# Kernel tuning notes

Hardware: AMD Instinct MI355X
Metric: run time of the kernel (lower is better)

## Reference

```python
import jax, jax.numpy as jnp
import numpy as np

N = 50000      # nodes
E = 800000     # edges (avg degree 16)
F_IN = 256
F_OUT = 256


def setup_inputs() -> dict:
    key = jax.random.key(0)
    ks = jax.random.split(key, 8)
    feature = jax.random.normal(ks[0], (N, F_IN), dtype=jnp.float32)
    e_w = jax.random.uniform(ks[1], (E, 1), dtype=jnp.float32)
    snorm_n = jnp.ones((N, 1), dtype=jnp.float32)
    snorm_e = jnp.ones((E, 1), dtype=jnp.float32)
    src = jax.random.randint(ks[2], (E,), 0, N, dtype=jnp.int32)
    dst = jax.random.randint(ks[3], (E,), 0, N, dtype=jnp.int32)
    scale = 1.0 / np.sqrt(F_IN)
    W_self = jax.random.normal(ks[4], (F_IN, F_OUT), dtype=jnp.float32) * scale
    W = jax.random.normal(ks[5], (F_IN, F_OUT), dtype=jnp.float32) * scale
    b = jax.random.normal(ks[6], (F_OUT,), dtype=jnp.float32) * scale
    return {"feature": feature, "e_w": e_w, "snorm_n": snorm_n,
            "snorm_e": snorm_e, "W_self": W_self, "W": W, "b": b,
            "src": src, "dst": dst}


def reference(feature, e_w, snorm_n, snorm_e, W_self, W, b, src, dst):
    n = feature.shape[0]
    ones_e = jnp.ones_like(src, dtype=feature.dtype)
    # self transform
    h_s = feature @ W_self                                   # [N, F_OUT]
    # source-side degree normalization: deg_out^{-1/2}
    out_deg = jnp.maximum(jax.ops.segment_sum(ones_e, src, num_segments=n), 1.0)
    feat = feature * (out_deg ** -0.5)[:, None]              # [N, F_IN]
    # message = h[src] * e_w, aggregated by sum into dst (u_mul_e + sum reduce)
    msgs = feat[src] * e_w                                   # [E, F_IN]
    agg = jax.ops.segment_sum(msgs, dst, num_segments=n)     # [N, F_IN]
    # neighbor transform + destination-side degree normalization
    h = agg @ W + b                                          # [N, F_OUT]
    in_deg = jnp.maximum(jax.ops.segment_sum(ones_e, dst, num_segments=n), 1.0)
    h = h * (in_deg ** -0.5)[:, None]
    return h_s + h, e_w
```

## Files before the change

### kernel.cpp

```cpp
#include <hip/hip_runtime.h>
#include <hip/hip_bf16.h>

#define N_NODES 50000
#define N_EDGES 800000
#define MP      50048
#define MAXDEG  64

#define PREP_A_BLOCKS 12512
#define EDGE_BLOCKS   3125
#define PREPW_BLOCKS  512

typedef __bf16 bf16x8_t __attribute__((ext_vector_type(8)));
typedef float  f32x4_t  __attribute__((ext_vector_type(4)));

__device__ __forceinline__ unsigned short f2bf(float x) {
  __hip_bfloat16 h = __float2bfloat16(x);
  return __builtin_bit_cast(unsigned short, h);
}
__device__ __forceinline__ float bf2f(unsigned short u) {
  unsigned int v = ((unsigned int)u) << 16;
  return __builtin_bit_cast(float, v);
}

__global__ __launch_bounds__(256) void prep_fused(
    const float* __restrict__ feature, const float* __restrict__ Wself,
    const float* __restrict__ W, const float* __restrict__ e_w,
    const int* __restrict__ src, const int* __restrict__ dst,
    unsigned short* __restrict__ Abf, unsigned short* __restrict__ Bt,
    int* __restrict__ cnt_in, int* __restrict__ cnt_out,
    unsigned int* __restrict__ bucket, float* __restrict__ out1)
{
  const int b = blockIdx.x, tid = threadIdx.x;
  if (b < PREP_A_BLOCKS) {
    int idx4 = b * 256 + tid;
    size_t base = (size_t)idx4 * 4;
    int row = (int)(base >> 8);
    ushort4 o;
    if (row < N_NODES) {
      const float4 v = *(const float4*)(feature + base);
      o.x = f2bf(v.x); o.y = f2bf(v.y); o.z = f2bf(v.z); o.w = f2bf(v.w);
    } else {
      o.x = o.y = o.z = o.w = 0;
    }
    *(ushort4*)(Abf + base) = o;
  } else if (b < PREP_A_BLOCKS + EDGE_BLOCKS) {
    int e = (b - PREP_A_BLOCKS) * 256 + tid;
    if (e < N_EDGES) {
      int s = src[e];
      int d = dst[e];
      float w = e_w[e];
      out1[e] = w;
      atomicAdd(&cnt_out[s], 1);
      int p = atomicAdd(&cnt_in[d], 1);
      if (p < MAXDEG) {
        unsigned int ent = ((unsigned int)f2bf(w) << 16) | (unsigned int)s;
        bucket[(size_t)d * MAXDEG + p] = ent;
      }
    }
  } else {
    int idx = (b - (PREP_A_BLOCKS + EDGE_BLOCKS)) * 256 + tid;
    int n = idx >> 8, k = idx & 255;
    float v = (n < 256) ? Wself[k * 256 + n] : W[k * 256 + (n - 256)];
    Bt[idx] = f2bf(v);
  }
}

__global__ __launch_bounds__(256, 2) void gemm_kernel(
    const unsigned short* __restrict__ A,
    const unsigned short* __restrict__ Bt,
    const float* __restrict__ bias,
    const int* __restrict__ cnt_in,
    const int* __restrict__ cnt_out,
    float* __restrict__ out0,
    unsigned char* __restrict__ y8)
{
  __shared__ unsigned short As[2][128 * 32];
  __shared__ unsigned short Bs[2][256 * 32];
  const int tid  = threadIdx.x;
  const int lane = tid & 63;
  const int wave = tid >> 6;
  const int m0 = blockIdx.x * 128;
  const int n0 = blockIdx.y * 256;
  const int wm = (wave & 1) * 64;
  const int wn = (wave >> 1) * 128;
  const int fr = lane & 15;
  const int fk = (lane >> 4) * 8;
  const int srow  = lane >> 2;
  const int scolb = (lane & 3) * 8;

  f32x4_t acc[4][8] = {};

  for (int k0 = 0; k0 < 256; k0 += 64) {
#pragma unroll
    for (int p = 0; p < 2; ++p) {
      int kk = k0 + p * 32;
#pragma unroll
      for (int j = 0; j < 2; ++j) {
        int rr = wave * 32 + j * 16;
        const unsigned short* ga = A + (size_t)(m0 + rr + srow) * 256 + (kk + scolb);
        __builtin_amdgcn_global_load_lds((const __attribute__((address_space(1))) void*)ga,
                                         (__attribute__((address_space(3))) void*)&As[p][rr * 32],
                                         16, 0, 0);
      }
#pragma unroll
      for (int j = 0; j < 4; ++j) {
        int rr = wave * 64 + j * 16;
        const unsigned short* gb = Bt + (size_t)(n0 + rr + srow) * 256 + (kk + scolb);
        __builtin_amdgcn_global_load_lds((const __attribute__((address_space(1))) void*)gb,
                                         (__attribute__((address_space(3))) void*)&Bs[p][rr * 32],
                                         16, 0, 0);
      }
    }
    __syncthreads();

#pragma unroll
    for (int p = 0; p < 2; ++p) {
      bf16x8_t af[4], bfr[8];
#pragma unroll
      for (int i = 0; i < 4; ++i)
        af[i]  = *(const bf16x8_t*)&As[p][(wm + i * 16 + fr) * 32 + fk];
#pragma unroll
      for (int j = 0; j < 8; ++j)
        bfr[j] = *(const bf16x8_t*)&Bs[p][(wn + j * 16 + fr) * 32 + fk];
#pragma unroll
      for (int i = 0; i < 4; ++i)
#pragma unroll
        for (int j = 0; j < 8; ++j)
          acc[i][j] = __builtin_amdgcn_mfma_f32_16x16x32_bf16(af[i], bfr[j], acc[i][j], 0, 0, 0);
    }
    __syncthreads();
  }

  if (blockIdx.y == 0) {
#pragma unroll
    for (int i = 0; i < 4; ++i) {
      int rowb = m0 + wm + i * 16 + (lane >> 4) * 4;
      float indv[4];
#pragma unroll
      for (int r = 0; r < 4; ++r) {
        int row = rowb + r;
        if (row < N_NODES) {
          int ci = cnt_in[row]; if (ci < 1) ci = 1;
          indv[r] = rsqrtf((float)ci);
        } else indv[r] = 0.f;
      }
#pragma unroll
      for (int j = 0; j < 8; ++j) {
        int col = wn + j * 16 + (lane & 15);
        float bc = bias[col];
#pragma unroll
        for (int r = 0; r < 4; ++r) {
          int row = rowb + r;
          if (row < N_NODES)
            out0[(size_t)row * 256 + col] = acc[i][j][r] + bc * indv[r];
        }
      }
    }
  } else {
#pragma unroll
    for (int i = 0; i < 4; ++i) {
      int rowb = m0 + wm + i * 16 + (lane >> 4) * 4;
      float odv[4];
#pragma unroll
      for (int r = 0; r < 4; ++r) {
        int row = rowb + r;
        if (row < N_NODES) {
          int co = cnt_out[row]; if (co < 1) co = 1;
          odv[r] = rsqrtf((float)co);
        } else odv[r] = 0.f;
      }
#pragma unroll
      for (int j = 0; j < 8; ++j) {
        int col = wn + j * 16 + (lane & 15);
#pragma unroll
        for (int r = 0; r < 4; ++r) {
          int row = rowb + r;
          if (row < N_NODES) {
            float ys = acc[i][j][r] * odv[r];
            unsigned int pk = (unsigned int)__builtin_amdgcn_cvt_pk_fp8_f32(ys, ys, 0, false);
            y8[(size_t)row * 256 + col] = (unsigned char)(pk & 0xffu);
          }
        }
      }
    }
  }
}

__global__ __launch_bounds__(256) void agg_kernel(
    const unsigned char* __restrict__ y8, const unsigned int* __restrict__ bucket,
    const int* __restrict__ cnt_in, float* __restrict__ out0)
{
  const int wave = threadIdx.x >> 6, lane = threadIdx.x & 63;
  const int node = blockIdx.x * 4 + wave;
  if (node >= N_NODES) return;
  int deg_raw = cnt_in[node];
  int deg = deg_raw > MAXDEG ? MAXDEG : deg_raw;

  unsigned int ent = 0u;
  if (lane < deg) ent = bucket[(size_t)node * MAXDEG + lane];
  float wl = bf2f((unsigned short)(ent >> 16));
  int   sl = (int)(ent & 0xffffu);

  float a0 = 0.f, a1 = 0.f, a2 = 0.f, a3 = 0.f;
  for (int b = 0; b < MAXDEG; b += 16) {
    if (b >= deg) break;
#pragma unroll
    for (int t = 0; t < 16; ++t) {
      int eb = b + t;
      int   s = __shfl(sl, eb);
      float w = __shfl(wl, eb);
      bool ok = eb < deg;
      s = ok ? s : 0;
      w = ok ? w : 0.0f;
      unsigned int u = *(const unsigned int*)(y8 + (size_t)s * 256 + lane * 4);
      a0 += w * __builtin_amdgcn_cvt_f32_fp8(u, 0);
      a1 += w * __builtin_amdgcn_cvt_f32_fp8(u, 1);
      a2 += w * __builtin_amdgcn_cvt_f32_fp8(u, 2);
      a3 += w * __builtin_amdgcn_cvt_f32_fp8(u, 3);
    }
  }

  int dn = deg_raw < 1 ? 1 : deg_raw;
  float inv = rsqrtf((float)dn);
  float4 o = *(float4*)(out0 + (size_t)node * 256 + lane * 4);
  o.x += a0 * inv; o.y += a1 * inv; o.z += a2 * inv; o.w += a3 * inv;
  *(float4*)(out0 + (size_t)node * 256 + lane * 4) = o;
}

extern "C" void kernel_launch(void* const* d_in, const int* in_sizes, int n_in,
                              void* d_out, int out_size, void* d_ws, size_t ws_size,
                              hipStream_t stream) {
  const float* feature = (const float*)d_in[0];
  const float* e_w     = (const float*)d_in[1];
  const float* W_self  = (const float*)d_in[4];
  const float* W       = (const float*)d_in[5];
  const float* bias    = (const float*)d_in[6];
  const int*   src     = (const int*)d_in[7];
  const int*   dst     = (const int*)d_in[8];

  float* out0 = (float*)d_out;
  float* out1 = out0 + (size_t)N_NODES * 256;

  char* ws = (char*)d_ws;
  int*            cnt_in  = (int*)(ws + 0);
  int*            cnt_out = (int*)(ws + 204800);
  unsigned int*   bucket  = (unsigned int*)(ws + 409600);
  unsigned short* Bt      = (unsigned short*)(ws + 13209600);
  unsigned short* Abf     = (unsigned short*)(ws + 13471744);
  unsigned char*  y8      = (unsigned char*)(ws + 39096320);

  hipMemsetAsync(ws, 0, 409600, stream);

  prep_fused<<<PREP_A_BLOCKS + EDGE_BLOCKS + PREPW_BLOCKS, 256, 0, stream>>>(
      feature, W_self, W, e_w, src, dst, Abf, Bt, cnt_in, cnt_out, bucket, out1);
  gemm_kernel<<<dim3(MP / 128, 2), 256, 0, stream>>>(Abf, Bt, bias, cnt_in, cnt_out, out0, y8);
  agg_kernel<<<(N_NODES + 3) / 4, 256, 0, stream>>>(y8, bucket, cnt_in, out0);
}
```

Baseline: 264.2 us.

## Fuse feature bf16 conversion into GEMM and run edge pass in same launch

The separate pass that converts feature to bf16 is removed. The GEMM now loads fp32 feature rows directly into registers and converts them there. The edge bucketing pass runs as extra blocks of the same launch, so degree counting overlaps the GEMM. Because degrees are not final during the GEMM, the neighbor half is written unscaled as bf16, and a new scale_y8 kernel applies the out-degree scaling and fp8 packing; bias moves into the aggregation kernel. This saves the Abf write and reread but adds a bf16 intermediate pass, one extra launch and uncoalesced direct A loads.

```diff
diff --git a/kernel.cpp b/kernel.cpp
--- a/kernel.cpp
+++ b/kernel.cpp
@@ -6,12 +6,12 @@
 #define MP      50048
 #define MAXDEG  64
 
-#define PREP_A_BLOCKS 12512
-#define EDGE_BLOCKS   3125
-#define PREPW_BLOCKS  512
+#define EDGE_BLOCKS 3125
+#define GEMM_BLOCKS 782
 
 typedef __bf16 bf16x8_t __attribute__((ext_vector_type(8)));
 typedef float  f32x4_t  __attribute__((ext_vector_type(4)));
+typedef unsigned short ushort8_t __attribute__((ext_vector_type(8)));
 
 __device__ __forceinline__ unsigned short f2bf(float x) {
   __hip_bfloat16 h = __float2bfloat16(x);
@@ -22,65 +22,51 @@
   return __builtin_bit_cast(float, v);
 }
 
-__global__ __launch_bounds__(256) void prep_fused(
-    const float* __restrict__ feature, const float* __restrict__ Wself,
-    const float* __restrict__ W, const float* __restrict__ e_w,
+__global__ __launch_bounds__(256) void prep_W(
+    const float* __restrict__ Wself, const float* __restrict__ W,
+    unsigned short* __restrict__ Bt)
+{
+  int idx = blockIdx.x * 256 + threadIdx.x;
+  int n = idx >> 8, k = idx & 255;
+  float v = (n < 256) ? Wself[k * 256 + n] : W[k * 256 + (n - 256)];
+  Bt[idx] = f2bf(v);
+}
+
+__global__ __launch_bounds__(256, 2) void mega_kernel(
+    const float* __restrict__ feature,
+    const float* __restrict__ e_w,
     const int* __restrict__ src, const int* __restrict__ dst,
-    unsigned short* __restrict__ Abf, unsigned short* __restrict__ Bt,
+    const unsigned short* __restrict__ Bt,
     int* __restrict__ cnt_in, int* __restrict__ cnt_out,
-    unsigned int* __restrict__ bucket, float* __restrict__ out1)
-{
-  const int b = blockIdx.x, tid = threadIdx.x;
-  if (b < PREP_A_BLOCKS) {
-    int idx4 = b * 256 + tid;
-    size_t base = (size_t)idx4 * 4;
-    int row = (int)(base >> 8);
-    ushort4 o;
-    if (row < N_NODES) {
-      const float4 v = *(const float4*)(feature + base);
-      o.x = f2bf(v.x); o.y = f2bf(v.y); o.z = f2bf(v.z); o.w = f2bf(v.w);
-    } else {
-      o.x = o.y = o.z = o.w = 0;
-    }
-    *(ushort4*)(Abf + base) = o;
-  } else if (b < PREP_A_BLOCKS + EDGE_BLOCKS) {
-    int e = (b - PREP_A_BLOCKS) * 256 + tid;
-    if (e < N_EDGES) {
-      int s = src[e];
-      int d = dst[e];
-      float w = e_w[e];
-      out1[e] = w;
-      atomicAdd(&cnt_out[s], 1);
-      int p = atomicAdd(&cnt_in[d], 1);
-      if (p < MAXDEG) {
-        unsigned int ent = ((unsigned int)f2bf(w) << 16) | (unsigned int)s;
-        bucket[(size_t)d * MAXDEG + p] = ent;
-      }
-    }
-  } else {
-    int idx = (b - (PREP_A_BLOCKS + EDGE_BLOCKS)) * 256 + tid;
-    int n = idx >> 8, k = idx & 255;
-    float v = (n < 256) ? Wself[k * 256 + n] : W[k * 256 + (n - 256)];
-    Bt[idx] = f2bf(v);
-  }
-}
-
-__global__ __launch_bounds__(256, 2) void gemm_kernel(
-    const unsigned short* __restrict__ A,
-    const unsigned short* __restrict__ Bt,
-    const float* __restrict__ bias,
-    const int* __restrict__ cnt_in,
-    const int* __restrict__ cnt_out,
+    unsigned int* __restrict__ bucket, float* __restrict__ out1,
     float* __restrict__ out0,
-    unsigned char* __restrict__ y8)
-{
-  __shared__ unsigned short As[2][128 * 32];
+    unsigned short* __restrict__ zraw)
+{
+  const int bid = blockIdx.x;
+  const int tid = threadIdx.x;
+
+  if (bid < EDGE_BLOCKS) {
+    int e = bid * 256 + tid;
+    int s = src[e];
+    int d = dst[e];
+    float w = e_w[e];
+    out1[e] = w;
+    atomicAdd(&cnt_out[s], 1);
+    int p = atomicAdd(&cnt_in[d], 1);
+    if (p < MAXDEG) {
+      unsigned int ent = ((unsigned int)f2bf(w) << 16) | (unsigned int)s;
+      bucket[(size_t)d * MAXDEG + p] = ent;
+    }
+    return;
+  }
+
   __shared__ unsigned short Bs[2][256 * 32];
-  const int tid  = threadIdx.x;
+  const int gb = bid - EDGE_BLOCKS;
+  const int m0 = (gb >> 1) * 128;
+  const int nhalf = gb & 1;
+  const int n0 = nhalf * 256;
   const int lane = tid & 63;
   const int wave = tid >> 6;
-  const int m0 = blockIdx.x * 128;
-  const int n0 = blockIdx.y * 256;
   const int wm = (wave & 1) * 64;
   const int wn = (wave >> 1) * 128;
   const int fr = lane & 15;
@@ -95,30 +81,39 @@
     for (int p = 0; p < 2; ++p) {
       int kk = k0 + p * 32;
 #pragma unroll
-      for (int j = 0; j < 2; ++j) {
-        int rr = wave * 32 + j * 16;
-        const unsigned short* ga = A + (size_t)(m0 + rr + srow) * 256 + (kk + scolb);
-        __builtin_amdgcn_global_load_lds((const __attribute__((address_space(1))) void*)ga,
-                                         (__attribute__((address_space(3))) void*)&As[p][rr * 32],
-                                         16, 0, 0);
-      }
-#pragma unroll
       for (int j = 0; j < 4; ++j) {
         int rr = wave * 64 + j * 16;
-        const unsigned short* gb = Bt + (size_t)(n0 + rr + srow) * 256 + (kk + scolb);
-        __builtin_amdgcn_global_load_lds((const __attribute__((address_space(1))) void*)gb,
+        const unsigned short* gbp = Bt + (size_t)(n0 + rr + srow) * 256 + (kk + scolb);
+        __builtin_amdgcn_global_load_lds((const __attribute__((address_space(1))) void*)gbp,
                                          (__attribute__((address_space(3))) void*)&Bs[p][rr * 32],
                                          16, 0, 0);
       }
     }
+
+    bf16x8_t af[2][4];
+#pragma unroll
+    for (int p = 0; p < 2; ++p) {
+      int kk = k0 + p * 32;
+#pragma unroll
+      for (int i = 0; i < 4; ++i) {
+        int row = m0 + wm + i * 16 + fr;
+        const float* ap = feature + (size_t)row * 256 + kk + fk;
+        float4 lo = make_float4(0.f, 0.f, 0.f, 0.f), hi = lo;
+        if (row < N_NODES) {
+          lo = *(const float4*)ap;
+          hi = *(const float4*)(ap + 4);
+        }
+        ushort8_t u;
+        u[0] = f2bf(lo.x); u[1] = f2bf(lo.y); u[2] = f2bf(lo.z); u[3] = f2bf(lo.w);
+        u[4] = f2bf(hi.x); u[5] = f2bf(hi.y); u[6] = f2bf(hi.z); u[7] = f2bf(hi.w);
+        af[p][i] = __builtin_bit_cast(bf16x8_t, u);
+      }
+    }
     __syncthreads();
 
 #pragma unroll
     for (int p = 0; p < 2; ++p) {
-      bf16x8_t af[4], bfr[8];
-#pragma unroll
-      for (int i = 0; i < 4; ++i)
-        af[i]  = *(const bf16x8_t*)&As[p][(wm + i * 16 + fr) * 32 + fk];
+      bf16x8_t bfr[8];
 #pragma unroll
       for (int j = 0; j < 8; ++j)
         bfr[j] = *(const bf16x8_t*)&Bs[p][(wn + j * 16 + fr) * 32 + fk];
@@ -126,33 +121,23 @@
       for (int i = 0; i < 4; ++i)
 #pragma unroll
         for (int j = 0; j < 8; ++j)
-          acc[i][j] = __builtin_amdgcn_mfma_f32_16x16x32_bf16(af[i], bfr[j], acc[i][j], 0, 0, 0);
+          acc[i][j] = __builtin_amdgcn_mfma_f32_16x16x32_bf16(af[p][i], bfr[j], acc[i][j], 0, 0, 0);
     }
     __syncthreads();
   }
 
-  if (blockIdx.y == 0) {
+  if (nhalf == 0) {
 #pragma unroll
     for (int i = 0; i < 4; ++i) {
       int rowb = m0 + wm + i * 16 + (lane >> 4) * 4;
-      float indv[4];
-#pragma unroll
-      for (int r = 0; r < 4; ++r) {
-        int row = rowb + r;
-        if (row < N_NODES) {
-          int ci = cnt_in[row]; if (ci < 1) ci = 1;
-          indv[r] = rsqrtf((float)ci);
-        } else indv[r] = 0.f;
-      }
 #pragma unroll
       for (int j = 0; j < 8; ++j) {
         int col = wn + j * 16 + (lane & 15);
-        float bc = bias[col];
 #pragma unroll
         for (int r = 0; r < 4; ++r) {
           int row = rowb + r;
           if (row < N_NODES)
-            out0[(size_t)row * 256 + col] = acc[i][j][r] + bc * indv[r];
+            out0[(size_t)row * 256 + col] = acc[i][j][r];
         }
       }
     }
@@ -160,35 +145,51 @@
 #pragma unroll
     for (int i = 0; i < 4; ++i) {
       int rowb = m0 + wm + i * 16 + (lane >> 4) * 4;
-      float odv[4];
-#pragma unroll
-      for (int r = 0; r < 4; ++r) {
-        int row = rowb + r;
-        if (row < N_NODES) {
-          int co = cnt_out[row]; if (co < 1) co = 1;
-          odv[r] = rsqrtf((float)co);
-        } else odv[r] = 0.f;
-      }
 #pragma unroll
       for (int j = 0; j < 8; ++j) {
         int col = wn + j * 16 + (lane & 15);
 #pragma unroll
         for (int r = 0; r < 4; ++r) {
           int row = rowb + r;
-          if (row < N_NODES) {
-            float ys = acc[i][j][r] * odv[r];
-            unsigned int pk = (unsigned int)__builtin_amdgcn_cvt_pk_fp8_f32(ys, ys, 0, false);
-            y8[(size_t)row * 256 + col] = (unsigned char)(pk & 0xffu);
-          }
+          if (row < N_NODES)
+            zraw[(size_t)row * 256 + col] = f2bf(acc[i][j][r]);
         }
       }
     }
   }
+}
+
+__global__ __launch_bounds__(256) void scale_y8(
+    const unsigned short* __restrict__ zraw, const int* __restrict__ cnt_out,
+    unsigned char* __restrict__ y8)
+{
+  int idx = blockIdx.x * 256 + threadIdx.x;
+  int row = idx >> 4;
+  size_t eo = (size_t)idx * 16;
+  int co = cnt_out[row]; if (co < 1) co = 1;
+  float s = rsqrtf((float)co);
+  const ushort8_t* zp = (const ushort8_t*)(zraw + eo);
+  ushort8_t z0 = zp[0], z1 = zp[1];
+  float v[16];
+#pragma unroll
+  for (int t = 0; t < 8; ++t) { v[t] = bf2f(z0[t]) * s; v[8 + t] = bf2f(z1[t]) * s; }
+  uint4 o;
+  unsigned int d;
+  d = (unsigned int)__builtin_amdgcn_cvt_pk_fp8_f32(v[0],  v[1],  0u, false);
+  o.x = (unsigned int)__builtin_amdgcn_cvt_pk_fp8_f32(v[2],  v[3],  d,  true);
+  d = (unsigned int)__builtin_amdgcn_cvt_pk_fp8_f32(v[4],  v[5],  0u, false);
+  o.y = (unsigned int)__builtin_amdgcn_cvt_pk_fp8_f32(v[6],  v[7],  d,  true);
+  d = (unsigned int)__builtin_amdgcn_cvt_pk_fp8_f32(v[8],  v[9],  0u, false);
+  o.z = (unsigned int)__builtin_amdgcn_cvt_pk_fp8_f32(v[10], v[11], d,  true);
+  d = (unsigned int)__builtin_amdgcn_cvt_pk_fp8_f32(v[12], v[13], 0u, false);
+  o.w = (unsigned int)__builtin_amdgcn_cvt_pk_fp8_f32(v[14], v[15], d,  true);
+  *(uint4*)(y8 + eo) = o;
 }
 
 __global__ __launch_bounds__(256) void agg_kernel(
     const unsigned char* __restrict__ y8, const unsigned int* __restrict__ bucket,
-    const int* __restrict__ cnt_in, float* __restrict__ out0)
+    const int* __restrict__ cnt_in, const float* __restrict__ bias,
+    float* __restrict__ out0)
 {
   const int wave = threadIdx.x >> 6, lane = threadIdx.x & 63;
   const int node = blockIdx.x * 4 + wave;
@@ -222,8 +223,12 @@
 
   int dn = deg_raw < 1 ? 1 : deg_raw;
   float inv = rsqrtf((float)dn);
+  float4 bv = *(const float4*)(bias + lane * 4);
   float4 o = *(float4*)(out0 + (size_t)node * 256 + lane * 4);
-  o.x += a0 * inv; o.y += a1 * inv; o.z += a2 * inv; o.w += a3 * inv;
+  o.x += (a0 + bv.x) * inv;
+  o.y += (a1 + bv.y) * inv;
+  o.z += (a2 + bv.z) * inv;
+  o.w += (a3 + bv.w) * inv;
   *(float4*)(out0 + (size_t)node * 256 + lane * 4) = o;
 }
 
@@ -246,13 +251,14 @@
   int*            cnt_out = (int*)(ws + 204800);
   unsigned int*   bucket  = (unsigned int*)(ws + 409600);
   unsigned short* Bt      = (unsigned short*)(ws + 13209600);
-  unsigned short* Abf     = (unsigned short*)(ws + 13471744);
+  unsigned short* zraw    = (unsigned short*)(ws + 13471744);
   unsigned char*  y8      = (unsigned char*)(ws + 39096320);
 
   hipMemsetAsync(ws, 0, 409600, stream);
 
-  prep_fused<<<PREP_A_BLOCKS + EDGE_BLOCKS + PREPW_BLOCKS, 256, 0, stream>>>(
-      feature, W_self, W, e_w, src, dst, Abf, Bt, cnt_in, cnt_out, bucket, out1);
-  gemm_kernel<<<dim3(MP / 128, 2), 256, 0, stream>>>(Abf, Bt, bias, cnt_in, cnt_out, out0, y8);
-  agg_kernel<<<(N_NODES + 3) / 4, 256, 0, stream>>>(y8, bucket, cnt_in, out0);
-}
+  prep_W<<<512, 256, 0, stream>>>(W_self, W, Bt);
+  mega_kernel<<<EDGE_BLOCKS + GEMM_BLOCKS, 256, 0, stream>>>(
+      feature, e_w, src, dst, Bt, cnt_in, cnt_out, bucket, out1, out0, zraw);
+  scale_y8<<<3125, 256, 0, stream>>>(zraw, cnt_out, y8);
+  agg_kernel<<<(N_NODES + 3) / 4, 256, 0, stream>>>(y8, bucket, cnt_in, bias, out0);
+}
```

Measured after the change: 303.7 us. 14.9% more time.
